# Kernel tuning notes

Measured on AMD Instinct MI355X. Metric: run time of the kernel, lower is better.

Reference implementation:

```python
import jax, jax.numpy as jnp
import numpy as np

B, S, H, NH = 2, 2048, 768, 12
HD = H // NH  # 64
MAXPOS = 2048


def _rope_tables(max_pos, d):
    # bert4torch get_sinusoid_encoding_table: even cols sin, odd cols cos
    pos = np.arange(max_pos, dtype=np.float32)[:, None]
    div = np.exp(np.arange(0, d, 2, dtype=np.float32) * (-np.log(10000.0) / d))
    tab = np.zeros((max_pos, d), np.float32)
    tab[:, 0::2] = np.sin(pos * div)
    tab[:, 1::2] = np.cos(pos * div)
    cos = np.concatenate([tab[:, 1::2], tab[:, 1::2]], axis=1)  # [:,1::2].repeat(1,2)
    sin = np.concatenate([tab[:, 0::2], tab[:, 0::2]], axis=1)  # [:,0::2].repeat(1,2)
    return jnp.asarray(cos), jnp.asarray(sin)


def setup_inputs() -> dict:
    key = jax.random.key(0)
    ks = jax.random.split(key, 10)
    s = 0.02
    inp = {}
    inp["hidden_states"] = jax.random.normal(ks[0], (B, S, H), jnp.float32)
    inp["attention_mask"] = jnp.ones((B, 1, 1, S), jnp.float32)
    for i, n in enumerate(["q", "k", "v", "o"]):
        inp[f"W{n}"] = (jax.random.normal(ks[1 + i], (H, H), jnp.float32) * s)
        inp[f"b{n}"] = jnp.zeros((H,), jnp.float32)
    cos, sin = _rope_tables(MAXPOS, HD)
    inp["cos_position"] = cos
    inp["sin_position"] = sin
    return inp


def _apply_rope(qw, cos, sin):
    # Faithful to source: seq_len_dim defaults to 1, which on a
    # [B, heads, S, head_dim] tensor is the HEADS axis.
    L = qw.shape[1]
    qw2 = jnp.concatenate([-qw[..., 1::2], qw[..., 0::2]], axis=-1)
    return qw * cos[:L][None, :, None, :] + qw2 * sin[:L][None, :, None, :]


def reference(hidden_states, attention_mask, Wq, bq, Wk, bk, Wv, bv, Wo, bo,
              cos_position, sin_position):
    b, s, _ = hidden_states.shape

    def heads(x):  # [b,s,H] -> [b,NH,s,HD]
        return x.reshape(b, s, NH, HD).transpose(0, 2, 1, 3)

    q = heads(hidden_states @ Wq + bq)
    k = heads(hidden_states @ Wk + bk)
    v = heads(hidden_states @ Wv + bv)
    q = _apply_rope(q, cos_position, sin_position)
    k = _apply_rope(k, cos_position, sin_position)
    scores = jnp.einsum('bnid,bnjd->bnij', q, k) / jnp.sqrt(jnp.float32(HD))
    scores = scores + (1.0 - attention_mask) * (-10000.0)
    probs = jax.nn.softmax(scores, axis=-1)  # dropout is identity in eval
    ctx = jnp.einsum('bnij,bnjd->bnid', probs, v)
    ctx = ctx.transpose(0, 2, 1, 3).reshape(b, s, H)
    return ctx @ Wo + bo
```

## Files before the change

### kernel.cpp

```cpp
#include <hip/hip_runtime.h>

#define B 2
#define S 2048
#define H 768
#define NH 12
#define HD 64
#define BS (B * S)
#define LOG2E 1.4426950408889634f

typedef unsigned short u16;
typedef short short8 __attribute__((ext_vector_type(8)));
typedef float f32x4 __attribute__((ext_vector_type(4)));
typedef float f32x16 __attribute__((ext_vector_type(16)));

__device__ __forceinline__ u16 f2bf(float f) {
    union { float f; unsigned u; } c; c.f = f;
    unsigned u = c.u + 0x7FFFu + ((c.u >> 16) & 1u);
    return (u16)(u >> 16);
}
__device__ __forceinline__ float bf2f(u16 h) {
    union { unsigned u; float f; } c; c.u = ((unsigned)h) << 16;
    return c.f;
}
__device__ __forceinline__ f32x16 zero16() {
    f32x16 v;
    #pragma unroll
    for (int i = 0; i < 16; ++i) v[i] = 0.f;
    return v;
}

__device__ __forceinline__ void g2l16(const u16* g, u16* l) {
    __builtin_amdgcn_global_load_lds(
        (const __attribute__((address_space(1))) void*)g,
        (__attribute__((address_space(3))) void*)l, 16, 0, 0);
}

__global__ __launch_bounds__(256) void prep_kernel(
    const float* __restrict__ hs,
    const float* __restrict__ Wq, const float* __restrict__ Wk,
    const float* __restrict__ Wv, const float* __restrict__ Wo,
    const float* __restrict__ bq, const float* __restrict__ bk,
    const float* __restrict__ cosp, const float* __restrict__ sinp,
    u16* __restrict__ hsb, u16* __restrict__ WTqkv, u16* __restrict__ WTo,
    float* __restrict__ bqk2)
{
    __shared__ float Lt[64 * 65];
    const int bid = blockIdx.x;
    const int t = threadIdx.x;

    if (bid >= 576) {
        size_t i = ((size_t)(bid - 576) * 256 + t) * 8;
        float4 a = *(const float4*)(hs + i);
        float4 b = *(const float4*)(hs + i + 4);
        short8 p;
        p[0] = (short)f2bf(a.x); p[1] = (short)f2bf(a.y);
        p[2] = (short)f2bf(a.z); p[3] = (short)f2bf(a.w);
        p[4] = (short)f2bf(b.x); p[5] = (short)f2bf(b.y);
        p[6] = (short)f2bf(b.z); p[7] = (short)f2bf(b.w);
        *(short8*)(hsb + i) = p;
        return;
    }

    const int z   = bid / 144;
    const int rem = bid - z * 144;
    const int k0 = (rem / 12) * 64, n0 = (rem % 12) * 64;
    const float* W = (z == 0) ? Wq : (z == 1) ? Wk : (z == 2) ? Wv : Wo;
    u16* D = (z == 3) ? WTo : (WTqkv + (size_t)z * H * H);
    const int head = n0 >> 6;
    const float scl = (z == 0) ? (0.125f * LOG2E) : 1.0f;

    if (z < 2 && rem / 12 == 0 && t < 64) {
        const float* bs = (z == 0) ? bq : bk;
        int d = t;
        int pd = (d < 32) ? (2 * d + 1) : (2 * (d - 32));
        float sv = ((d < 32) ? -1.f : 1.f) * sinp[head * HD + d];
        float cv = cosp[head * HD + d];
        bqk2[z * H + n0 + d] = scl * (cv * bs[n0 + d] + sv * bs[n0 + pd]);
    }

    #pragma unroll
    for (int u = 0; u < 4; ++u) {
        int f = t + u * 256;
        int r = f >> 4, c4 = (f & 15) * 4;
        float4 w = *(const float4*)(W + (size_t)(k0 + r) * H + n0 + c4);
        Lt[r * 65 + c4 + 0] = w.x; Lt[r * 65 + c4 + 1] = w.y;
        Lt[r * 65 + c4 + 2] = w.z; Lt[r * 65 + c4 + 3] = w.w;
    }
    __syncthreads();
    #pragma unroll
    for (int u = 0; u < 4; ++u) {
        int f = t + u * 256;
        int n = f >> 4, k4 = (f & 15) * 4;
        ushort4 p;
        if (z < 2) {
            int pn = (n < 32) ? (2 * n + 1) : (2 * (n - 32));
            float cv = scl * cosp[head * HD + n];
            float sv = scl * ((n < 32) ? -1.f : 1.f) * sinp[head * HD + n];
            p.x = f2bf(cv * Lt[(k4 + 0) * 65 + n] + sv * Lt[(k4 + 0) * 65 + pn]);
            p.y = f2bf(cv * Lt[(k4 + 1) * 65 + n] + sv * Lt[(k4 + 1) * 65 + pn]);
            p.z = f2bf(cv * Lt[(k4 + 2) * 65 + n] + sv * Lt[(k4 + 2) * 65 + pn]);
            p.w = f2bf(cv * Lt[(k4 + 3) * 65 + n] + sv * Lt[(k4 + 3) * 65 + pn]);
        } else {
            p.x = f2bf(Lt[(k4 + 0) * 65 + n]);
            p.y = f2bf(Lt[(k4 + 1) * 65 + n]);
            p.z = f2bf(Lt[(k4 + 2) * 65 + n]);
            p.w = f2bf(Lt[(k4 + 3) * 65 + n]);
        }
        *(ushort4*)(D + (size_t)(n0 + n) * H + k0 + k4) = p;
    }
}

__global__ __launch_bounds__(256) void gemm_qkv_kernel(
    const u16* __restrict__ A, const u16* __restrict__ BT,
    const float* __restrict__ bqk2, const float* __restrict__ bv,
    u16* __restrict__ Qb, u16* __restrict__ Kb, u16* __restrict__ VT)
{
    __shared__ alignas(16) u16 Abuf[2][128 * 64];
    __shared__ alignas(16) u16 Bbuf[2][128 * 64];

    const int tid  = threadIdx.x;
    const int w    = tid >> 6;
    const int lane = tid & 63;
    const int quad = lane >> 4;
    const int l15  = lane & 15;
    const int wm = (w & 1) * 64, wn = (w >> 1) * 64;
    const int m0 = (blockIdx.x & 31) * 128;
    const int n0 = (blockIdx.x >> 5) * 128;
    const int NK = H / 64;

    int srow[4], slc[4];
    #pragma unroll
    for (int u = 0; u < 4; ++u) {
        int s = u * 256 + tid;
        srow[u] = s >> 3;
        slc[u]  = (s & 7) ^ (srow[u] & 7);
    }

    #define QSTAGE(IT, NB)                                                    \
        _Pragma("unroll")                                                     \
        for (int u = 0; u < 4; ++u) {                                         \
            g2l16(A  + (size_t)(m0 + srow[u]) * H + (IT) * 64 + slc[u] * 8,   \
                  &Abuf[NB][(u * 256 + w * 64) * 8]);                         \
            g2l16(BT + (size_t)(n0 + srow[u]) * H + (IT) * 64 + slc[u] * 8,   \
                  &Bbuf[NB][(u * 256 + w * 64) * 8]);                         \
        }

    QSTAGE(0, 0)

    f32x4 acc[4][4];
    #pragma unroll
    for (int i = 0; i < 4; ++i)
        #pragma unroll
        for (int j = 0; j < 4; ++j) acc[i][j] = (f32x4){0.f, 0.f, 0.f, 0.f};

    for (int it = 0; it < NK; ++it) {
        const int cur = it & 1;
        __syncthreads();
        if (it + 1 < NK) { QSTAGE(it + 1, cur ^ 1) }

        const u16* Ac = Abuf[cur];
        const u16* Bc = Bbuf[cur];
        #pragma unroll
        for (int kc = 0; kc < 2; ++kc) {
            const int ch = kc * 4 + quad;
            short8 af[4], bf[4];
            #pragma unroll
            for (int mi = 0; mi < 4; ++mi) {
                int row = wm + mi * 16 + l15;
                af[mi] = *(const short8*)&Ac[row * 64 + (ch ^ (row & 7)) * 8];
            }
            #pragma unroll
            for (int ni = 0; ni < 4; ++ni) {
                int row = wn + ni * 16 + l15;
                bf[ni] = *(const short8*)&Bc[row * 64 + (ch ^ (row & 7)) * 8];
            }
            #pragma unroll
            for (int mi = 0; mi < 4; ++mi)
                #pragma unroll
                for (int ni = 0; ni < 4; ++ni)
                    acc[mi][ni] = __builtin_amdgcn_mfma_f32_16x16x32_bf16(
                        af[mi], bf[ni], acc[mi][ni], 0, 0, 0);
        }
    }
    #undef QSTAGE

    #pragma unroll
    for (int mi = 0; mi < 4; ++mi) {
        const int mbase = m0 + wm + mi * 16 + quad * 4;
        #pragma unroll
        for (int ni = 0; ni < 4; ++ni) {
            const int col = n0 + wn + ni * 16 + l15;
            const int which = col / H;
            const int c = col - which * H;
            const int h = c >> 6, d = c & 63;
            if (which == 2) {
                const float bias = bv[c];
                const int b_ = mbase >> 11, s = mbase & (S - 1);
                ushort4 pk;
                pk.x = f2bf(acc[mi][ni][0] + bias);
                pk.y = f2bf(acc[mi][ni][1] + bias);
                pk.z = f2bf(acc[mi][ni][2] + bias);
                pk.w = f2bf(acc[mi][ni][3] + bias);
                *(ushort4*)&VT[(((size_t)b_ * NH + h) * HD + d) * S + s] = pk;
            } else {
                u16* dst = (which == 0) ? Qb : Kb;
                const float bias = bqk2[which * H + c];
                #pragma unroll
                for (int r = 0; r < 4; ++r) {
                    int m = mbase + r;
                    int b_ = m >> 11, s = m & (S - 1);
                    dst[(((size_t)b_ * NH + h) * S + s) * HD + d] =
                        f2bf(acc[mi][ni][r] + bias);
                }
            }
        }
    }
}

__global__ __launch_bounds__(256) void gemm_out_kernel(
    const u16* __restrict__ A, const u16* __restrict__ BT,
    const float* __restrict__ bo, float* __restrict__ out)
{
    __shared__ alignas(16) u16 Abuf[2][128 * 64];
    __shared__ alignas(16) u16 Bbuf[2][64 * 64];

    const int tid  = threadIdx.x;
    const int w    = tid >> 6;
    const int lane = tid & 63;
    const int quad = lane >> 4;
    const int l15  = lane & 15;
    const int wm = (w & 1) * 64, wn = (w >> 1) * 32;
    const int m0 = (blockIdx.x & 31) * 128;
    const int n0 = (blockIdx.x >> 5) * 64;
    const int NK = H / 64;

    int srow[4], slc[4];
    #pragma unroll
    for (int u = 0; u < 4; ++u) {
        int s = u * 256 + tid;
        srow[u] = s >> 3;
        slc[u]  = (s & 7) ^ (srow[u] & 7);
    }

    #define OSTAGE(IT, NB)                                                    \
        _Pragma("unroll")                                                     \
        for (int u = 0; u < 4; ++u)                                           \
            g2l16(A + (size_t)(m0 + srow[u]) * H + (IT) * 64 + slc[u] * 8,    \
                  &Abuf[NB][(u * 256 + w * 64) * 8]);                         \
        _Pragma("unroll")                                                     \
        for (int u = 0; u < 2; ++u)                                           \
            g2l16(BT + (size_t)(n0 + srow[u]) * H + (IT) * 64 + slc[u] * 8,   \
                  &Bbuf[NB][(u * 256 + w * 64) * 8]);

    OSTAGE(0, 0)

    f32x4 acc[4][2];
    #pragma unroll
    for (int i = 0; i < 4; ++i)
        #pragma unroll
        for (int j = 0; j < 2; ++j) acc[i][j] = (f32x4){0.f, 0.f, 0.f, 0.f};

    for (int it = 0; it < NK; ++it) {
        const int cur = it & 1;
        __syncthreads();
        if (it + 1 < NK) { OSTAGE(it + 1, cur ^ 1) }

        const u16* Ac = Abuf[cur];
        const u16* Bc = Bbuf[cur];
        #pragma unroll
        for (int kc = 0; kc < 2; ++kc) {
            const int ch = kc * 4 + quad;
            short8 af[4], bf[2];
            #pragma unroll
            for (int mi = 0; mi < 4; ++mi) {
                int row = wm + mi * 16 + l15;
                af[mi] = *(const short8*)&Ac[row * 64 + (ch ^ (row & 7)) * 8];
            }
            #pragma unroll
            for (int ni = 0; ni < 2; ++ni) {
                int row = wn + ni * 16 + l15;
                bf[ni] = *(const short8*)&Bc[row * 64 + (ch ^ (row & 7)) * 8];
            }
            #pragma unroll
            for (int mi = 0; mi < 4; ++mi)
                #pragma unroll
                for (int ni = 0; ni < 2; ++ni)
                    acc[mi][ni] = __builtin_amdgcn_mfma_f32_16x16x32_bf16(
                        af[mi], bf[ni], acc[mi][ni], 0, 0, 0);
        }
    }
    #undef OSTAGE

    #pragma unroll
    for (int mi = 0; mi < 4; ++mi) {
        const int mbase = m0 + wm + mi * 16 + quad * 4;
        #pragma unroll
        for (int ni = 0; ni < 2; ++ni) {
            const int col = n0 + wn + ni * 16 + l15;
            const float bias = bo[col];
            #pragma unroll
            for (int r = 0; r < 4; ++r)
                out[(size_t)(mbase + r) * H + col] = acc[mi][ni][r] + bias;
        }
    }
}

__global__ __launch_bounds__(256) void attn_mfma_kernel(
    const u16* __restrict__ Q, const u16* __restrict__ K,
    const u16* __restrict__ VT, const float* __restrict__ mask,
    u16* __restrict__ ctx)
{
    __shared__ alignas(16) u16 smem[21504];
    u16* const Kbase = smem;
    u16* const Vbase = smem + 8192;
    u16* const Psw   = smem + 16384 + (threadIdx.x >> 6) * 1280;

    const int tid  = threadIdx.x;
    const int w    = tid >> 6;
    const int lane = tid & 63;
    const int l31  = lane & 31;
    const int h5   = lane >> 5;
    const int rh   = w & 1;
    const int kh   = w >> 1;
    const int bid = blockIdx.x;
    const int bn = bid % 24;
    const int q0 = (bid / 24) * 64;
    const int b = bn / NH, hh = bn % NH;
    const int NT = S / 64;

    short8 qa[4];
    {
        const u16* Qp = Q + ((size_t)bn * S + q0 + rh * 32 + l31) * HD + h5 * 8;
        #pragma unroll
        for (int kc = 0; kc < 4; ++kc)
            qa[kc] = *(const short8*)(Qp + kc * 16);
    }

    const u16* Kg = K + (size_t)bn * S * HD;
    const u16* Vg = VT + (size_t)bn * HD * S;
    const float* mrow = mask + (size_t)b * S;

    int srow[2], slc[2];
    #pragma unroll
    for (int u = 0; u < 2; ++u) {
        int s = u * 256 + tid;
        srow[u] = s >> 3;
        slc[u]  = (s & 7) ^ (srow[u] & 7);
    }

    #define STAGE(JT, NB)                                                     \
        _Pragma("unroll")                                                     \
        for (int u = 0; u < 2; ++u) {                                         \
            g2l16(Kg + (size_t)((JT) * 64 + srow[u]) * HD + slc[u] * 8,       \
                  Kbase + (NB) * 4096 + (u * 256 + w * 64) * 8);              \
            g2l16(Vg + (size_t)srow[u] * S + (JT) * 64 + slc[u] * 8,          \
                  Vbase + (NB) * 4096 + (u * 256 + w * 64) * 8);              \
        }

    STAGE(0, 0)

    f32x16 o0 = zero16(), o1 = zero16();
    float l_p[16];
    #pragma unroll
    for (int i = 0; i < 16; ++i) l_p[i] = 0.f;

    for (int jt = 0; jt < NT; ++jt) {
        const int cur = jt & 1;
        const float mv = mrow[jt * 64 + kh * 32 + l31];
        __syncthreads();
        if (jt + 1 < NT) { STAGE(jt + 1, cur ^ 1) }

        const u16* Kc = Kbase + cur * 4096;
        const u16* Vc = Vbase + cur * 4096;

        f32x16 sc = zero16();
        {
            const int krow = kh * 32 + l31;
            const int sw = krow & 7;
            #pragma unroll
            for (int kc = 0; kc < 4; ++kc) {
                const short8 kb =
                    *(const short8*)&Kc[krow * 64 + ((kc * 2 + h5) ^ sw) * 8];
                sc = __builtin_amdgcn_mfma_f32_32x32x16_bf16(qa[kc], kb, sc, 0, 0, 0);
            }
        }

        short8 vb[2][2];
        #pragma unroll
        for (int nt = 0; nt < 2; ++nt) {
            const int vrow = nt * 32 + l31;
            const int sw = vrow & 7;
            vb[nt][0] = *(const short8*)&Vc[vrow * 64 + ((kh * 4 + h5) ^ sw) * 8];
            vb[nt][1] = *(const short8*)&Vc[vrow * 64 + ((kh * 4 + 2 + h5) ^ sw) * 8];
        }

        const float mt = (1.0f - mv) * (-10000.0f * LOG2E);
        #pragma unroll
        for (int reg = 0; reg < 16; ++reg) {
            float p = __builtin_amdgcn_exp2f(sc[reg] + mt);
            l_p[reg] += p;
            const int r32 = (reg & 3) + 8 * (reg >> 2) + 4 * h5;
            Psw[r32 * 40 + l31] = f2bf(p);
        }

        asm volatile("s_waitcnt lgkmcnt(0)" ::: "memory");

        const short8 pa0 = *(const short8*)&Psw[l31 * 40 + h5 * 8];
        const short8 pa1 = *(const short8*)&Psw[l31 * 40 + 16 + h5 * 8];

        o0 = __builtin_amdgcn_mfma_f32_32x32x16_bf16(pa0, vb[0][0], o0, 0, 0, 0);
        o0 = __builtin_amdgcn_mfma_f32_32x32x16_bf16(pa1, vb[0][1], o0, 0, 0, 0);
        o1 = __builtin_amdgcn_mfma_f32_32x32x16_bf16(pa0, vb[1][0], o1, 0, 0, 0);
        o1 = __builtin_amdgcn_mfma_f32_32x32x16_bf16(pa1, vb[1][1], o1, 0, 0, 0);
    }
    #undef STAGE

    #pragma unroll
    for (int reg = 0; reg < 16; ++reg) {
        #pragma unroll
        for (int off = 16; off >= 1; off >>= 1)
            l_p[reg] += __shfl_xor(l_p[reg], off, 32);
    }

    __syncthreads();
    float* cb = (float*)smem;
    float* lb = (float*)(smem + 16384);

    if (kh == 1) {
        float* c = cb + rh * 2048;
        #pragma unroll
        for (int reg = 0; reg < 16; ++reg) {
            float2 v = make_float2(o0[reg], o1[reg]);
            *(float2*)&c[reg * 128 + lane * 2] = v;
        }
        if (l31 == 0) {
            #pragma unroll
            for (int reg = 0; reg < 16; ++reg)
                lb[rh * 32 + h5 * 16 + reg] = l_p[reg];
        }
    }
    __syncthreads();
    if (kh == 0) {
        const float* c = cb + rh * 2048;
        #pragma unroll
        for (int reg = 0; reg < 16; ++reg) {
            float2 po = *(const float2*)&c[reg * 128 + lane * 2];
            float lt = l_p[reg] + lb[rh * 32 + h5 * 16 + reg];
            float inv = 1.0f / lt;
            const int r32 = (reg & 3) + 8 * (reg >> 2) + 4 * h5;
            const int s = q0 + rh * 32 + r32;
            u16* dst = ctx + ((size_t)b * S + s) * H + hh * 64;
            dst[l31]      = f2bf((o0[reg] + po.x) * inv);
            dst[32 + l31] = f2bf((o1[reg] + po.y) * inv);
        }
    }
}

extern "C" void kernel_launch(void* const* d_in, const int* in_sizes, int n_in,
                              void* d_out, int out_size, void* d_ws, size_t ws_size,
                              hipStream_t stream)
{
    const float* hs   = (const float*)d_in[0];
    const float* mask = (const float*)d_in[1];
    const float* Wq   = (const float*)d_in[2];
    const float* bq   = (const float*)d_in[3];
    const float* Wk   = (const float*)d_in[4];
    const float* bk   = (const float*)d_in[5];
    const float* Wv   = (const float*)d_in[6];
    const float* bv   = (const float*)d_in[7];
    const float* Wo   = (const float*)d_in[8];
    const float* bo   = (const float*)d_in[9];
    const float* cosp = (const float*)d_in[10];
    const float* sinp = (const float*)d_in[11];
    float* out = (float*)d_out;

    const size_t per = (size_t)B * NH * S * HD;
    u16* ws    = (u16*)d_ws;
    u16* hsb   = ws;
    u16* WTqkv = hsb + per;
    u16* WTo   = WTqkv + (size_t)3 * H * H;
    u16* Qb    = WTo + (size_t)H * H;
    u16* Kb    = Qb + per;
    u16* VT    = Kb + per;
    u16* ctxb  = VT + per;
    float* bqk2 = (float*)(ctxb + per);

    prep_kernel<<<576 + (BS * H) / 2048, 256, 0, stream>>>(
        hs, Wq, Wk, Wv, Wo, bq, bk, cosp, sinp, hsb, WTqkv, WTo, bqk2);

    gemm_qkv_kernel<<<(BS / 128) * (2304 / 128), 256, 0, stream>>>(
        hsb, WTqkv, bqk2, bv, Qb, Kb, VT);

    attn_mfma_kernel<<<(S / 64) * (B * NH), 256, 0, stream>>>(
        Qb, Kb, VT, mask, ctxb);

    gemm_out_kernel<<<(BS / 128) * (H / 64), 256, 0, stream>>>(
        ctxb, WTo, bo, out);
}
```

Measured before the change: 192.6 us.

## Transpose attention MFMAs to keep P in registers and fold mask via MFMA

Swaps the operand order of the QK^T and PV MFMAs, so the score tile lands transposed and each lane holds one query row's probabilities. This lets P be repacked to bf16 with a lane-xor-32 shuffle instead of a per-wave LDS round trip and waitcnt. It also seeds the score accumulator with the mask bias through an MFMA against a one-hot vector. The row-sum becomes a per-lane scalar, which removes the 16-register cross-lane reduction, and the epilogue writes packed ushort4 stores. The costs are an extra MFMA per tile and the mask bias being rounded to bf16.

Result: faster. 188.7 us (-2.0%).

```diff
diff --git a/kernel.cpp b/kernel.cpp
--- a/kernel.cpp
+++ b/kernel.cpp
@@ -9,6 +9,7 @@
 #define LOG2E 1.4426950408889634f
 
 typedef unsigned short u16;
+typedef unsigned int u32;
 typedef short short8 __attribute__((ext_vector_type(8)));
 typedef float f32x4 __attribute__((ext_vector_type(4)));
 typedef float f32x16 __attribute__((ext_vector_type(16)));
@@ -28,6 +29,7 @@
     for (int i = 0; i < 16; ++i) v[i] = 0.f;
     return v;
 }
+union pk4 { uint4 u; short8 s; };
 
 __device__ __forceinline__ void g2l16(const u16* g, u16* l) {
     __builtin_amdgcn_global_load_lds(
@@ -313,7 +315,6 @@
     __shared__ alignas(16) u16 smem[21504];
     u16* const Kbase = smem;
     u16* const Vbase = smem + 8192;
-    u16* const Psw   = smem + 16384 + (threadIdx.x >> 6) * 1280;
 
     const int tid  = threadIdx.x;
     const int w    = tid >> 6;
@@ -336,6 +337,9 @@
             qa[kc] = *(const short8*)(Qp + kc * 16);
     }
 
+    short8 oneb = {};
+    if (h5 == 0) oneb[0] = (short)0x3F80;
+
     const u16* Kg = K + (size_t)bn * S * HD;
     const u16* Vg = VT + (size_t)bn * HD * S;
     const float* mrow = mask + (size_t)b * S;
@@ -360,9 +364,7 @@
     STAGE(0, 0)
 
     f32x16 o0 = zero16(), o1 = zero16();
-    float l_p[16];
-    #pragma unroll
-    for (int i = 0; i < 16; ++i) l_p[i] = 0.f;
+    float l_acc = 0.f;
 
     for (int jt = 0; jt < NT; ++jt) {
         const int cur = jt & 1;
@@ -373,7 +375,12 @@
         const u16* Kc = Kbase + cur * 4096;
         const u16* Vc = Vbase + cur * 4096;
 
-        f32x16 sc = zero16();
+        const float mt = (1.0f - mv) * (-10000.0f * LOG2E);
+        short8 mta = {};
+        if (h5 == 0) mta[0] = (short)f2bf(mt);
+        f32x16 sc = __builtin_amdgcn_mfma_f32_32x32x16_bf16(
+            mta, oneb, zero16(), 0, 0, 0);
+
         {
             const int krow = kh * 32 + l31;
             const int sw = krow & 7;
@@ -381,77 +388,88 @@
             for (int kc = 0; kc < 4; ++kc) {
                 const short8 kb =
                     *(const short8*)&Kc[krow * 64 + ((kc * 2 + h5) ^ sw) * 8];
-                sc = __builtin_amdgcn_mfma_f32_32x32x16_bf16(qa[kc], kb, sc, 0, 0, 0);
+                sc = __builtin_amdgcn_mfma_f32_32x32x16_bf16(kb, qa[kc], sc, 0, 0, 0);
             }
         }
 
-        short8 vb[2][2];
+        short8 va[2][2];
         #pragma unroll
         for (int nt = 0; nt < 2; ++nt) {
             const int vrow = nt * 32 + l31;
             const int sw = vrow & 7;
-            vb[nt][0] = *(const short8*)&Vc[vrow * 64 + ((kh * 4 + h5) ^ sw) * 8];
-            vb[nt][1] = *(const short8*)&Vc[vrow * 64 + ((kh * 4 + 2 + h5) ^ sw) * 8];
-        }
-
-        const float mt = (1.0f - mv) * (-10000.0f * LOG2E);
-        #pragma unroll
-        for (int reg = 0; reg < 16; ++reg) {
-            float p = __builtin_amdgcn_exp2f(sc[reg] + mt);
-            l_p[reg] += p;
-            const int r32 = (reg & 3) + 8 * (reg >> 2) + 4 * h5;
-            Psw[r32 * 40 + l31] = f2bf(p);
-        }
-
-        asm volatile("s_waitcnt lgkmcnt(0)" ::: "memory");
-
-        const short8 pa0 = *(const short8*)&Psw[l31 * 40 + h5 * 8];
-        const short8 pa1 = *(const short8*)&Psw[l31 * 40 + 16 + h5 * 8];
-
-        o0 = __builtin_amdgcn_mfma_f32_32x32x16_bf16(pa0, vb[0][0], o0, 0, 0, 0);
-        o0 = __builtin_amdgcn_mfma_f32_32x32x16_bf16(pa1, vb[0][1], o0, 0, 0, 0);
-        o1 = __builtin_amdgcn_mfma_f32_32x32x16_bf16(pa0, vb[1][0], o1, 0, 0, 0);
-        o1 = __builtin_amdgcn_mfma_f32_32x32x16_bf16(pa1, vb[1][1], o1, 0, 0, 0);
+            va[nt][0] = *(const short8*)&Vc[vrow * 64 + ((kh * 4 + h5) ^ sw) * 8];
+            va[nt][1] = *(const short8*)&Vc[vrow * 64 + ((kh * 4 + 2 + h5) ^ sw) * 8];
+        }
+
+        float p[16];
+        #pragma unroll
+        for (int r = 0; r < 16; ++r) {
+            p[r] = __builtin_amdgcn_exp2f(sc[r]);
+            l_acc += p[r];
+        }
+        u32 d[8];
+        #pragma unroll
+        for (int i = 0; i < 8; ++i)
+            d[i] = ((u32)f2bf(p[2 * i + 1]) << 16) | (u32)f2bf(p[2 * i]);
+
+        u32 e0 = h5 ? d[0] : d[2];
+        u32 e1 = h5 ? d[1] : d[3];
+        u32 e2 = h5 ? d[4] : d[6];
+        u32 e3 = h5 ? d[5] : d[7];
+        u32 r0 = (u32)__shfl_xor((int)e0, 32, 64);
+        u32 r1 = (u32)__shfl_xor((int)e1, 32, 64);
+        u32 r2 = (u32)__shfl_xor((int)e2, 32, 64);
+        u32 r3 = (u32)__shfl_xor((int)e3, 32, 64);
+
+        pk4 f0, f1;
+        if (h5) {
+            f0.u = make_uint4(r0, r1, d[2], d[3]);
+            f1.u = make_uint4(r2, r3, d[6], d[7]);
+        } else {
+            f0.u = make_uint4(d[0], d[1], r0, r1);
+            f1.u = make_uint4(d[4], d[5], r2, r3);
+        }
+
+        o0 = __builtin_amdgcn_mfma_f32_32x32x16_bf16(va[0][0], f0.s, o0, 0, 0, 0);
+        o0 = __builtin_amdgcn_mfma_f32_32x32x16_bf16(va[0][1], f1.s, o0, 0, 0, 0);
+        o1 = __builtin_amdgcn_mfma_f32_32x32x16_bf16(va[1][0], f0.s, o1, 0, 0, 0);
+        o1 = __builtin_amdgcn_mfma_f32_32x32x16_bf16(va[1][1], f1.s, o1, 0, 0, 0);
     }
     #undef STAGE
 
-    #pragma unroll
-    for (int reg = 0; reg < 16; ++reg) {
-        #pragma unroll
-        for (int off = 16; off >= 1; off >>= 1)
-            l_p[reg] += __shfl_xor(l_p[reg], off, 32);
-    }
+    l_acc += __shfl_xor(l_acc, 32, 64);
 
     __syncthreads();
     float* cb = (float*)smem;
     float* lb = (float*)(smem + 16384);
 
     if (kh == 1) {
-        float* c = cb + rh * 2048;
-        #pragma unroll
-        for (int reg = 0; reg < 16; ++reg) {
-            float2 v = make_float2(o0[reg], o1[reg]);
-            *(float2*)&c[reg * 128 + lane * 2] = v;
-        }
-        if (l31 == 0) {
-            #pragma unroll
-            for (int reg = 0; reg < 16; ++reg)
-                lb[rh * 32 + h5 * 16 + reg] = l_p[reg];
-        }
+        #pragma unroll
+        for (int r = 0; r < 16; ++r) {
+            cb[r * 128 + rh * 64 + lane]        = o0[r];
+            cb[(16 + r) * 128 + rh * 64 + lane] = o1[r];
+        }
+        if (h5 == 0) lb[rh * 32 + l31] = l_acc;
     }
     __syncthreads();
     if (kh == 0) {
-        const float* c = cb + rh * 2048;
-        #pragma unroll
-        for (int reg = 0; reg < 16; ++reg) {
-            float2 po = *(const float2*)&c[reg * 128 + lane * 2];
-            float lt = l_p[reg] + lb[rh * 32 + h5 * 16 + reg];
-            float inv = 1.0f / lt;
-            const int r32 = (reg & 3) + 8 * (reg >> 2) + 4 * h5;
-            const int s = q0 + rh * 32 + r32;
-            u16* dst = ctx + ((size_t)b * S + s) * H + hh * 64;
-            dst[l31]      = f2bf((o0[reg] + po.x) * inv);
-            dst[32 + l31] = f2bf((o1[reg] + po.y) * inv);
+        float lt = l_acc + lb[rh * 32 + l31];
+        float inv = 1.0f / lt;
+        const int s = q0 + rh * 32 + l31;
+        u16* dst = ctx + ((size_t)b * S + s) * H + hh * 64;
+        #pragma unroll
+        for (int g = 0; g < 4; ++g) {
+            ushort4 pk0, pk1;
+            pk0.x = f2bf((o0[4 * g + 0] + cb[(4 * g + 0) * 128 + rh * 64 + lane]) * inv);
+            pk0.y = f2bf((o0[4 * g + 1] + cb[(4 * g + 1) * 128 + rh * 64 + lane]) * inv);
+            pk0.z = f2bf((o0[4 * g + 2] + cb[(4 * g + 2) * 128 + rh * 64 + lane]) * inv);
+            pk0.w = f2bf((o0[4 * g + 3] + cb[(4 * g + 3) * 128 + rh * 64 + lane]) * inv);
+            *(ushort4*)(dst + 8 * g + 4 * h5) = pk0;
+            pk1.x = f2bf((o1[4 * g + 0] + cb[(16 + 4 * g + 0) * 128 + rh * 64 + lane]) * inv);
+            pk1.y = f2bf((o1[4 * g + 1] + cb[(16 + 4 * g + 1) * 128 + rh * 64 + lane]) * inv);
+            pk1.z = f2bf((o1[4 * g + 2] + cb[(16 + 4 * g + 2) * 128 + rh * 64 + lane]) * inv);
+            pk1.w = f2bf((o1[4 * g + 3] + cb[(16 + 4 * g + 3) * 128 + rh * 64 + lane]) * inv);
+            *(ushort4*)(dst + 32 + 8 * g + 4 * h5) = pk1;
         }
     }
 }
```
